# Kernel optimization log

Measured on AMD Instinct MI355X. Metric: run time of the kernel, lower is better.

## Reference

```python
import jax, jax.numpy as jnp
import numpy as np

EPS = 1e-6


def setup_inputs() -> dict:
    key = jax.random.key(0)
    kx, kw = jax.random.split(key)
    B, C, N = 8, 256, 2048
    x = jax.random.normal(kx, (B, C, N), dtype=jnp.float32)
    # nn.Linear(dim*2, 2, bias=False): weight shape [2, 2*C]
    W = jax.random.normal(kw, (2, 2 * C), dtype=jnp.float32) * (1.0 / np.sqrt(2 * C))
    return {"x": x, "W": W}


def reference(x, W):
    B, C, N = x.shape
    # cosine similarity matrix [B, N, N]
    sim = jnp.einsum('bcn,bcm->bnm', x, x)
    # torch: sqrt(sum(x^2 + 1e-6, dim=1)) -> eps added per-channel before sum
    norms = jnp.sqrt(jnp.sum(x * x + EPS, axis=1))            # [B, N]
    io_abs = sim / (norms[:, :, None] * norms[:, None, :])    # [B, N, N]
    # zero the diagonal (fill_diagonal_(0)) before argmax
    io_abs = io_abs * (1.0 - jnp.eye(N, dtype=io_abs.dtype))
    idx = jnp.argmax(io_abs, axis=2)                          # [B, N] nearest-neighbor per token
    # gather retrieved features: f_re[b, :, n] = x[b, :, idx[b, n]]
    f_re = jnp.take_along_axis(x, idx[:, None, :], axis=2)    # [B, C, N]
    # gated fusion
    fus = jnp.concatenate([x, f_re], axis=1).transpose(0, 2, 1)  # [B, N, 2C]
    w = jax.nn.softmax(fus @ W.T, axis=-1)                    # [B, N, 2]
    w = w.transpose(0, 2, 1)                                  # [B, 2, N]
    out = x * w[:, 0:1, :] + f_re * w[:, 1:2, :]
    return (out, f_re)
```

## Files before the change

kernel.cpp:

```cpp
#include <hip/hip_runtime.h>
#include <hip/hip_bf16.h>
#include <math.h>

constexpr int B_ = 8;
constexpr int C_ = 256;
constexpr int N_ = 2048;
constexpr int CN_ = C_ * N_;
constexpr int TOT_ = B_ * C_ * N_;
constexpr int NTILES = 16;
constexpr int NPAIRS = 136;
constexpr float EPSC = 256.0f * 1e-6f;

typedef __attribute__((ext_vector_type(8))) short bf16x8;
typedef __attribute__((ext_vector_type(4))) float f32x4;

__device__ __forceinline__ void g2l16(const void* g, void* l) {
    __builtin_amdgcn_global_load_lds(
        (const __attribute__((address_space(1))) void*)g,
        (__attribute__((address_space(3))) void*)l, 16, 0, 0);
}

__device__ __forceinline__ unsigned short bits(__hip_bfloat16 h) {
    union { __hip_bfloat16 b; unsigned short u; } cv;
    cv.b = h;
    return cv.u;
}

__device__ __forceinline__ float b2f(short s) {
    union { float f; unsigned u; } cv;
    cv.u = ((unsigned)(unsigned short)s) << 16;
    return cv.f;
}

__device__ __forceinline__ unsigned long long packkey(float v, int m) {
    const unsigned b = __float_as_uint(v);
    const unsigned u = (b & 0x80000000u) ? ~b : (b | 0x80000000u);
    return ((unsigned long long)u << 32) | (unsigned)(2047 - m);
}

__global__ __launch_bounds__(256) void convert_kernel(const float* __restrict__ x,
                                                      __hip_bfloat16* __restrict__ hiT,
                                                      __hip_bfloat16* __restrict__ loT,
                                                      float* __restrict__ normacc) {
    const int blk = blockIdx.x;
    const int batch = blk & 7;
    const int nt = (blk >> 3) & 31;
    const int ctile = blk >> 8;
    const int n0 = nt << 6, c0 = ctile << 6;
    const int t = threadIdx.x;
    const int i = t & 63, j = t >> 6;

    __shared__ float tb[64][65];
    __shared__ float red[4][64];

    float s = 0.f;
    const float* xp = x + (size_t)batch * CN_ + (size_t)c0 * N_ + n0 + i;
#pragma unroll 4
    for (int r = 0; r < 16; ++r) {
        const int cl = j + r * 4;
        const float v = xp[(size_t)cl * N_];
        tb[cl][i] = v;
        s += v * v;
    }
    red[j][i] = s;
    __syncthreads();

    const int cp = t & 31;
    const int c2 = cp << 1;
    const int nb = t >> 5;
#pragma unroll 4
    for (int r = 0; r < 8; ++r) {
        const int n = nb + r * 8;
        const float v0 = tb[c2][n], v1 = tb[c2 + 1][n];
        const size_t o = ((size_t)batch * N_ + n0 + n) * C_ + c0 + c2;
        const __hip_bfloat16 h0 = __float2bfloat16(v0);
        const __hip_bfloat16 h1 = __float2bfloat16(v1);
        const __hip_bfloat16 g0 = __float2bfloat16(v0 - __bfloat162float(h0));
        const __hip_bfloat16 g1 = __float2bfloat16(v1 - __bfloat162float(h1));
        ((unsigned*)hiT)[o >> 1] = ((unsigned)bits(h1) << 16) | bits(h0);
        ((unsigned*)loT)[o >> 1] = ((unsigned)bits(g1) << 16) | bits(g0);
    }
    if (j == 0) {
        const float tt = red[0][i] + red[1][i] + red[2][i] + red[3][i];
        atomicAdd(normacc + batch * N_ + n0 + i, tt);
    }
}

__global__ __launch_bounds__(512) void gram_mfma_kernel(
        const __hip_bfloat16* __restrict__ hiT, const __hip_bfloat16* __restrict__ loT,
        const float* __restrict__ normacc,
        float* __restrict__ pval, int* __restrict__ pidx, float* __restrict__ pval2) {
    const int blk = blockIdx.x;
    const int batch = blk & 7;
    int p = blk >> 3;
    int bn = 0;
    while (p >= NTILES - bn) { p -= NTILES - bn; ++bn; }
    const int bm = bn + p;
    const bool diag = (bn == bm);
    const int n0 = bn << 7, m0 = bm << 7;

    __shared__ short As[128 * 64];
    __shared__ short Bs[128 * 64];
    short* ov = &As[0];
    float (*rv1)[4] = (float(*)[4])(ov + 0);
    int (*ri1)[4] = (int(*)[4])(ov + 1024);
    float (*rv2)[4] = (float(*)[4])(ov + 2048);
    float (*cv1)[2] = (float(*)[2])(ov + 3072);
    int (*ci1)[2] = (int(*)[2])(ov + 3584);
    float (*cv2)[2] = (float(*)[2])(ov + 4096);
    float* rnA = (float*)(ov + 4608);

    const int tid = threadIdx.x;
    const int l = tid & 63, w = tid >> 6;
    const int lm = l & 15, q = l >> 4;
    const int x7 = lm & 7;
    const int wn = (w >> 2) << 6;
    const int wm = (w & 3) << 5;

    const size_t bbase = (size_t)batch * CN_;
    const short* gA[2];
    const short* gB[2];
    int ldsoff[2];
#pragma unroll
    for (int pp = 0; pp < 2; ++pp) {
        const int slot = tid + pp * 512;
        const int r = slot >> 3, sidx = slot & 7;
        const int sw = sidx ^ (r & 7);
        const short* base = (const short*)((sw < 4) ? hiT : loT);
        gA[pp] = base + bbase + (size_t)(n0 + r) * C_ + (sw & 3) * 8;
        gB[pp] = base + bbase + (size_t)(m0 + r) * C_ + (sw & 3) * 8;
        ldsoff[pp] = slot * 8;
    }
    int aoff[8], boff[4];
#pragma unroll
    for (int rt = 0; rt < 4; ++rt) {
        const int ra = wn + rt * 16 + lm;
        aoff[rt * 2] = ra * 64 + ((q ^ x7) * 8);
        aoff[rt * 2 + 1] = ra * 64 + (((4 | q) ^ x7) * 8);
    }
#pragma unroll
    for (int ct = 0; ct < 2; ++ct) {
        const int rb = wm + ct * 16 + lm;
        boff[ct * 2] = rb * 64 + ((q ^ x7) * 8);
        boff[ct * 2 + 1] = rb * 64 + (((4 | q) ^ x7) * 8);
    }

    f32x4 acc[4][2];
#pragma unroll
    for (int rt = 0; rt < 4; ++rt)
#pragma unroll
        for (int ct = 0; ct < 2; ++ct) acc[rt][ct] = (f32x4){0.f, 0.f, 0.f, 0.f};

    for (int kt = 0; kt < 8; ++kt) {
        __syncthreads();
#pragma unroll
        for (int pp = 0; pp < 2; ++pp) {
            g2l16(gA[pp] + kt * 32, As + ldsoff[pp]);
            g2l16(gB[pp] + kt * 32, Bs + ldsoff[pp]);
        }
        __syncthreads();
        bf16x8 ah[4], al[4], bh[2], bl[2];
#pragma unroll
        for (int rt = 0; rt < 4; ++rt) {
            ah[rt] = *(const bf16x8*)(As + aoff[rt * 2]);
            al[rt] = *(const bf16x8*)(As + aoff[rt * 2 + 1]);
        }
#pragma unroll
        for (int ct = 0; ct < 2; ++ct) {
            bh[ct] = *(const bf16x8*)(Bs + boff[ct * 2]);
            bl[ct] = *(const bf16x8*)(Bs + boff[ct * 2 + 1]);
        }
#pragma unroll
        for (int rt = 0; rt < 4; ++rt)
#pragma unroll
            for (int ct = 0; ct < 2; ++ct) {
                acc[rt][ct] = __builtin_amdgcn_mfma_f32_16x16x32_bf16(
                    ah[rt], bh[ct], acc[rt][ct], 0, 0, 0);
                acc[rt][ct] = __builtin_amdgcn_mfma_f32_16x16x32_bf16(
                    ah[rt], bl[ct], acc[rt][ct], 0, 0, 0);
                acc[rt][ct] = __builtin_amdgcn_mfma_f32_16x16x32_bf16(
                    al[rt], bh[ct], acc[rt][ct], 0, 0, 0);
            }
    }
    __syncthreads();

    if (tid < 128) rnA[tid] = 1.0f / sqrtf(normacc[batch * N_ + n0 + tid] + EPSC);

    float rnm[2];
#pragma unroll
    for (int ct = 0; ct < 2; ++ct)
        rnm[ct] = 1.0f / sqrtf(normacc[batch * N_ + m0 + wm + ct * 16 + lm] + EPSC);

#pragma unroll
    for (int rt = 0; rt < 4; ++rt) {
#pragma unroll
        for (int r = 0; r < 4; ++r) {
            const int nrow = n0 + wn + rt * 16 + q * 4 + r;
            float v1 = -3.4e38f, v2 = -3.4e38f;
            int i1 = 0x7fffffff;
#pragma unroll
            for (int ct = 0; ct < 2; ++ct) {
                const int m = m0 + wm + ct * 16 + lm;
                const float v = acc[rt][ct][r] * rnm[ct];
                if (m == nrow) continue;
                if (v > v1) { v2 = v1; v1 = v; i1 = m; }
                else if (v > v2) v2 = v;
            }
#pragma unroll
            for (int d = 1; d < 16; d <<= 1) {
                const float ov1 = __shfl_xor(v1, d, 64);
                const int oi1 = __shfl_xor(i1, d, 64);
                const float ov2 = __shfl_xor(v2, d, 64);
                if (ov1 > v1 || (ov1 == v1 && oi1 < i1)) {
                    v2 = fmaxf(v1, ov2); v1 = ov1; i1 = oi1;
                } else {
                    v2 = fmaxf(v2, ov1);
                }
            }
            if (lm == 0) {
                const int rloc = wn + rt * 16 + q * 4 + r;
                rv1[rloc][w & 3] = v1;
                ri1[rloc][w & 3] = i1;
                rv2[rloc][w & 3] = v2;
            }
        }
    }
    __syncthreads();

    if (!diag) {
        float rnn[4][4];
#pragma unroll
        for (int rt = 0; rt < 4; ++rt)
#pragma unroll
            for (int r = 0; r < 4; ++r) rnn[rt][r] = rnA[wn + rt * 16 + q * 4 + r];
#pragma unroll
        for (int ct = 0; ct < 2; ++ct) {
            float v1 = -3.4e38f, v2 = -3.4e38f;
            int i1 = 0x7fffffff;
#pragma unroll
            for (int rt = 0; rt < 4; ++rt) {
#pragma unroll
                for (int r = 0; r < 4; ++r) {
                    const float v = acc[rt][ct][r] * rnn[rt][r];
                    const int nn = n0 + wn + rt * 16 + q * 4 + r;
                    if (v > v1) { v2 = v1; v1 = v; i1 = nn; }
                    else if (v > v2) v2 = v;
                }
            }
#pragma unroll
            for (int d = 16; d < 64; d <<= 1) {
                const float ov1 = __shfl_xor(v1, d, 64);
                const int oi1 = __shfl_xor(i1, d, 64);
                const float ov2 = __shfl_xor(v2, d, 64);
                if (ov1 > v1 || (ov1 == v1 && oi1 < i1)) {
                    v2 = fmaxf(v1, ov2); v1 = ov1; i1 = oi1;
                } else {
                    v2 = fmaxf(v2, ov1);
                }
            }
            if (q == 0) {
                const int mloc = wm + ct * 16 + lm;
                cv1[mloc][w >> 2] = v1;
                ci1[mloc][w >> 2] = i1;
                cv2[mloc][w >> 2] = v2;
            }
        }
    }
    __syncthreads();

    if (tid < 128) {
        {
            float v1 = rv1[tid][0]; int i1 = ri1[tid][0]; float v2 = rv2[tid][0];
#pragma unroll
            for (int s = 1; s < 4; ++s) {
                const float ov1 = rv1[tid][s]; const int oi1 = ri1[tid][s]; const float ov2 = rv2[tid][s];
                if (ov1 > v1 || (ov1 == v1 && oi1 < i1)) { v2 = fmaxf(v1, ov2); v1 = ov1; i1 = oi1; }
                else v2 = fmaxf(v2, ov1);
            }
            const size_t gi = (size_t)(batch * NTILES + bm) * N_ + n0 + tid;
            pval[gi] = v1; pidx[gi] = i1; pval2[gi] = v2;
        }
        if (!diag) {
            float v1 = cv1[tid][0]; int i1 = ci1[tid][0]; float v2 = cv2[tid][0];
            const float ov1 = cv1[tid][1]; const int oi1 = ci1[tid][1]; const float ov2 = cv2[tid][1];
            if (ov1 > v1 || (ov1 == v1 && oi1 < i1)) { v2 = fmaxf(v1, ov2); v1 = ov1; i1 = oi1; }
            else v2 = fmaxf(v2, ov1);
            const size_t gi = (size_t)(batch * NTILES + bn) * N_ + m0 + tid;
            pval[gi] = v1; pidx[gi] = i1; pval2[gi] = v2;
        }
    }
}

__global__ void combine_kernel(const float* __restrict__ pval, const int* __restrict__ pidx,
                               const float* __restrict__ pval2, int* __restrict__ fidx,
                               int* __restrict__ rcnt, int* __restrict__ ridx,
                               unsigned long long* __restrict__ pbest) {
    const int t = blockIdx.x * 256 + threadIdx.x;
    const int batch = t >> 11, n = t & 2047;
    float v1 = -3.4e38f, v2 = -3.4e38f;
    int i1 = 0x7fffffff;
    for (int s = 0; s < NTILES; ++s) {
        const size_t gi = (size_t)(batch * NTILES + s) * N_ + n;
        const float ov1 = pval[gi]; const int oi1 = pidx[gi]; const float ov2 = pval2[gi];
        if (ov1 > v1 || (ov1 == v1 && oi1 < i1)) { v2 = fmaxf(v1, ov2); v1 = ov1; i1 = oi1; }
        else v2 = fmaxf(v2, ov1);
    }
    fidx[t] = i1;
    if (v1 - v2 < 1e-4f) {
        const int slot = atomicAdd(rcnt, 1);
        ridx[slot] = t;
        pbest[slot] = 0ull;
    }
}

__global__ __launch_bounds__(256) void rescue_kernel(const float* __restrict__ x,
                                                     const float* __restrict__ normacc,
                                                     const int* __restrict__ rcnt,
                                                     const int* __restrict__ ridx,
                                                     unsigned long long* __restrict__ pbest) {
    const int cnt = *rcnt;
    const int nwork = cnt << 3;
    const int tid = threadIdx.x;
    __shared__ unsigned long long bk[256];
    for (int wi = blockIdx.x; wi < nwork; wi += gridDim.x) {
        const int rr = wi >> 3, ch = wi & 7;
        const int t = ridx[rr];
        const int batch = t >> 11, n = t & 2047;
        const int m = (ch << 8) + tid;
        const float* xb = x + (size_t)batch * CN_;
        float s0 = 0.f, s1 = 0.f, s2 = 0.f, s3 = 0.f;
        const float* xn = xb + n;
        const float* xm = xb + m;
#pragma unroll 4
        for (int c = 0; c < C_; c += 4) {
            s0 += xn[(size_t)(c + 0) * N_] * xm[(size_t)(c + 0) * N_];
            s1 += xn[(size_t)(c + 1) * N_] * xm[(size_t)(c + 1) * N_];
            s2 += xn[(size_t)(c + 2) * N_] * xm[(size_t)(c + 2) * N_];
            s3 += xn[(size_t)(c + 3) * N_] * xm[(size_t)(c + 3) * N_];
        }
        const float rn = 1.0f / sqrtf(normacc[batch * N_ + m] + EPSC);
        const float v = ((s0 + s1) + (s2 + s3)) * rn;
        bk[tid] = (m == n) ? 0ull : packkey(v, m);
        __syncthreads();
        for (int sft = 128; sft > 0; sft >>= 1) {
            if (tid < sft) {
                const unsigned long long o = bk[tid + sft];
                if (o > bk[tid]) bk[tid] = o;
            }
            __syncthreads();
        }
        if (tid == 0) atomicMax(&pbest[rr], bk[0]);
        __syncthreads();
    }
}

__global__ void rescue_fin_kernel(const unsigned long long* __restrict__ pbest,
                                  const int* __restrict__ rcnt,
                                  const int* __restrict__ ridx,
                                  int* __restrict__ fidx) {
    const int rr = blockIdx.x * 256 + threadIdx.x;
    if (rr < *rcnt) {
        const unsigned long long k = pbest[rr];
        const int m = 2047 - (int)(unsigned)(k & 0xffffffffull);
        fidx[ridx[rr]] = m;
    }
}

__global__ __launch_bounds__(512) void finish_kernel(const float* __restrict__ x,
                                                     const __hip_bfloat16* __restrict__ hiT,
                                                     const __hip_bfloat16* __restrict__ loT,
                                                     const float* __restrict__ W,
                                                     const int* __restrict__ fidx,
                                                     float* __restrict__ out) {
    const int batch = blockIdx.x & 7;
    const int nt = blockIdx.x >> 3;
    const int n0 = nt << 6;
    const int t = threadIdx.x;
    const int lane = t & 63, cw = t >> 6;

    __shared__ float Wl[1024];
    __shared__ int il[64];
    __shared__ float pl0[8][64], pl1[8][64];
    __shared__ float w0s[64], w1s[64];

    for (int u = t; u < 1024; u += 512) Wl[u] = W[u];
    if (t < 64) il[t] = fidx[batch * N_ + n0 + t];
    __syncthreads();

    const int myrow = il[lane];
    const size_t rowb = ((size_t)batch * N_ + myrow) * C_ + cw * 32;

    float fre[32];
    {
        const bf16x8* hp = (const bf16x8*)(hiT + rowb);
        const bf16x8* lp = (const bf16x8*)(loT + rowb);
#pragma unroll
        for (int v8 = 0; v8 < 4; ++v8) {
            const bf16x8 h = hp[v8];
            const bf16x8 g = lp[v8];
#pragma unroll
            for (int e = 0; e < 8; ++e) fre[v8 * 8 + e] = b2f(h[e]) + b2f(g[e]);
        }
    }

    const float* xb = x + (size_t)batch * CN_ + n0 + lane;
    float xr[32];
    float l0 = 0.f, l1 = 0.f;
#pragma unroll
    for (int cc = 0; cc < 32; ++cc) {
        const int c = cw * 32 + cc;
        const float xv = xb[(size_t)c * N_];
        xr[cc] = xv;
        l0 += xv * Wl[c] + fre[cc] * Wl[256 + c];
        l1 += xv * Wl[512 + c] + fre[cc] * Wl[768 + c];
    }
    pl0[cw][lane] = l0;
    pl1[cw][lane] = l1;
    __syncthreads();
    if (t < 64) {
        float L0 = 0.f, L1 = 0.f;
#pragma unroll
        for (int g = 0; g < 8; ++g) { L0 += pl0[g][t]; L1 += pl1[g][t]; }
        const float mx = fmaxf(L0, L1);
        const float e0 = expf(L0 - mx);
        const float e1 = expf(L1 - mx);
        const float inv = 1.0f / (e0 + e1);
        w0s[t] = e0 * inv;
        w1s[t] = e1 * inv;
    }
    __syncthreads();
    const float w0 = w0s[lane], w1 = w1s[lane];

#pragma unroll
    for (int cc = 0; cc < 32; ++cc) {
        const int c = cw * 32 + cc;
        const size_t off = (size_t)batch * CN_ + (size_t)c * N_ + n0 + lane;
        out[off] = xr[cc] * w0 + fre[cc] * w1;
        out[TOT_ + off] = fre[cc];
    }
}

extern "C" void kernel_launch(void* const* d_in, const int* in_sizes, int n_in,
                              void* d_out, int out_size, void* d_ws, size_t ws_size,
                              hipStream_t stream) {
    const float* x = (const float*)d_in[0];
    const float* W = (const float*)d_in[1];
    float* out = (float*)d_out;

    const size_t BF_BYTES = (size_t)TOT_ * 2;
    const size_t NORM_BYTES = (size_t)B_ * N_ * 4;
    const size_t P_BYTES = (size_t)B_ * NTILES * N_ * 4;

    uint8_t* p = (uint8_t*)d_ws;
    __hip_bfloat16* hiT = (__hip_bfloat16*)p; p += BF_BYTES;
    __hip_bfloat16* loT = (__hip_bfloat16*)p; p += BF_BYTES;
    float* normacc = (float*)p; p += NORM_BYTES;
    float* pval = (float*)p; p += P_BYTES;
    int* pidx = (int*)p; p += P_BYTES;
    float* pval2 = (float*)p; p += P_BYTES;
    int* fidx = (int*)p; p += NORM_BYTES;
    int* rcnt = (int*)p; p += 256;
    int* ridx = (int*)p; p += NORM_BYTES;
    unsigned long long* pbest = (unsigned long long*)p; p += (size_t)B_ * N_ * 8;

    hipMemsetAsync(rcnt, 0, 4, stream);
    hipMemsetAsync(normacc, 0, NORM_BYTES, stream);
    convert_kernel<<<1024, 256, 0, stream>>>(x, hiT, loT, normacc);
    gram_mfma_kernel<<<B_ * NPAIRS, 512, 0, stream>>>(hiT, loT, normacc, pval, pidx, pval2);
    combine_kernel<<<64, 256, 0, stream>>>(pval, pidx, pval2, fidx, rcnt, ridx, pbest);
    rescue_kernel<<<256, 256, 0, stream>>>(x, normacc, rcnt, ridx, pbest);
    rescue_fin_kernel<<<64, 256, 0, stream>>>(pbest, rcnt, ridx, fidx);
    finish_kernel<<<256, 512, 0, stream>>>(x, hiT, loT, W, fidx, out);
}
```

Baseline: 184.0 us.

## Double-buffer gram LDS tiles, drop memsets and atomics, fuse rescue finish

The gram kernel now double-buffers its A/B LDS tiles, prefetching the next k-slice while the current one feeds the MFMAs, and needs one barrier per iteration instead of two. Norm partial sums are written per channel tile into four slices and summed by the readers, which removes the atomicAdd and the memset of the accumulator. The rescue counter is zeroed inside convert_kernel instead of by a memset. The rescue_fin kernel is folded into finish_kernel, which scans the rescue list to patch its local indices. Together this cuts two memsets and one launch, at the cost of doubled LDS use (possible occupancy loss) and a per-block scan of the rescue list.

After: 174.2 us. -5.3%, faster.

```diff
diff --git a/kernel.cpp b/kernel.cpp
--- a/kernel.cpp
+++ b/kernel.cpp
@@ -7,6 +7,7 @@
 constexpr int N_ = 2048;
 constexpr int CN_ = C_ * N_;
 constexpr int TOT_ = B_ * C_ * N_;
+constexpr int BN_ = B_ * N_;
 constexpr int NTILES = 16;
 constexpr int NPAIRS = 136;
 constexpr float EPSC = 256.0f * 1e-6f;
@@ -38,10 +39,16 @@
     return ((unsigned long long)u << 32) | (unsigned)(2047 - m);
 }
 
+__device__ __forceinline__ float rnorm4(const float* __restrict__ normp, int idx) {
+    return 1.0f / sqrtf(normp[idx] + normp[BN_ + idx] + normp[2 * BN_ + idx] +
+                        normp[3 * BN_ + idx] + EPSC);
+}
+
 __global__ __launch_bounds__(256) void convert_kernel(const float* __restrict__ x,
                                                       __hip_bfloat16* __restrict__ hiT,
                                                       __hip_bfloat16* __restrict__ loT,
-                                                      float* __restrict__ normacc) {
+                                                      float* __restrict__ normp,
+                                                      int* __restrict__ rcnt) {
     const int blk = blockIdx.x;
     const int batch = blk & 7;
     const int nt = (blk >> 3) & 31;
@@ -49,6 +56,8 @@
     const int n0 = nt << 6, c0 = ctile << 6;
     const int t = threadIdx.x;
     const int i = t & 63, j = t >> 6;
+
+    if (blk == 0 && t == 0) rcnt[0] = 0;
 
     __shared__ float tb[64][65];
     __shared__ float red[4][64];
@@ -82,13 +91,13 @@
     }
     if (j == 0) {
         const float tt = red[0][i] + red[1][i] + red[2][i] + red[3][i];
-        atomicAdd(normacc + batch * N_ + n0 + i, tt);
+        normp[ctile * BN_ + batch * N_ + n0 + i] = tt;
     }
 }
 
 __global__ __launch_bounds__(512) void gram_mfma_kernel(
         const __hip_bfloat16* __restrict__ hiT, const __hip_bfloat16* __restrict__ loT,
-        const float* __restrict__ normacc,
+        const float* __restrict__ normp,
         float* __restrict__ pval, int* __restrict__ pidx, float* __restrict__ pval2) {
     const int blk = blockIdx.x;
     const int batch = blk & 7;
@@ -99,9 +108,11 @@
     const bool diag = (bn == bm);
     const int n0 = bn << 7, m0 = bm << 7;
 
-    __shared__ short As[128 * 64];
-    __shared__ short Bs[128 * 64];
-    short* ov = &As[0];
+    __shared__ short As0[128 * 64];
+    __shared__ short As1[128 * 64];
+    __shared__ short Bs0[128 * 64];
+    __shared__ short Bs1[128 * 64];
+    short* ov = &As0[0];
     float (*rv1)[4] = (float(*)[4])(ov + 0);
     int (*ri1)[4] = (int(*)[4])(ov + 1024);
     float (*rv2)[4] = (float(*)[4])(ov + 2048);
@@ -151,24 +162,36 @@
 #pragma unroll
         for (int ct = 0; ct < 2; ++ct) acc[rt][ct] = (f32x4){0.f, 0.f, 0.f, 0.f};
 
+#pragma unroll
+    for (int pp = 0; pp < 2; ++pp) {
+        g2l16(gA[pp], As0 + ldsoff[pp]);
+        g2l16(gB[pp], Bs0 + ldsoff[pp]);
+    }
+    __syncthreads();
+
+#pragma unroll
     for (int kt = 0; kt < 8; ++kt) {
-        __syncthreads();
-#pragma unroll
-        for (int pp = 0; pp < 2; ++pp) {
-            g2l16(gA[pp] + kt * 32, As + ldsoff[pp]);
-            g2l16(gB[pp] + kt * 32, Bs + ldsoff[pp]);
-        }
-        __syncthreads();
+        short* Ac = (kt & 1) ? As1 : As0;
+        short* Bc = (kt & 1) ? Bs1 : Bs0;
+        if (kt < 7) {
+            short* An = (kt & 1) ? As0 : As1;
+            short* Bn = (kt & 1) ? Bs0 : Bs1;
+#pragma unroll
+            for (int pp = 0; pp < 2; ++pp) {
+                g2l16(gA[pp] + (kt + 1) * 32, An + ldsoff[pp]);
+                g2l16(gB[pp] + (kt + 1) * 32, Bn + ldsoff[pp]);
+            }
+        }
         bf16x8 ah[4], al[4], bh[2], bl[2];
 #pragma unroll
         for (int rt = 0; rt < 4; ++rt) {
-            ah[rt] = *(const bf16x8*)(As + aoff[rt * 2]);
-            al[rt] = *(const bf16x8*)(As + aoff[rt * 2 + 1]);
+            ah[rt] = *(const bf16x8*)(Ac + aoff[rt * 2]);
+            al[rt] = *(const bf16x8*)(Ac + aoff[rt * 2 + 1]);
         }
 #pragma unroll
         for (int ct = 0; ct < 2; ++ct) {
-            bh[ct] = *(const bf16x8*)(Bs + boff[ct * 2]);
-            bl[ct] = *(const bf16x8*)(Bs + boff[ct * 2 + 1]);
+            bh[ct] = *(const bf16x8*)(Bc + boff[ct * 2]);
+            bl[ct] = *(const bf16x8*)(Bc + boff[ct * 2 + 1]);
         }
 #pragma unroll
         for (int rt = 0; rt < 4; ++rt)
@@ -181,15 +204,15 @@
                 acc[rt][ct] = __builtin_amdgcn_mfma_f32_16x16x32_bf16(
                     al[rt], bh[ct], acc[rt][ct], 0, 0, 0);
             }
-    }
-    __syncthreads();
-
-    if (tid < 128) rnA[tid] = 1.0f / sqrtf(normacc[batch * N_ + n0 + tid] + EPSC);
+        __syncthreads();
+    }
+
+    if (tid < 128) rnA[tid] = rnorm4(normp, batch * N_ + n0 + tid);
 
     float rnm[2];
 #pragma unroll
     for (int ct = 0; ct < 2; ++ct)
-        rnm[ct] = 1.0f / sqrtf(normacc[batch * N_ + m0 + wm + ct * 16 + lm] + EPSC);
+        rnm[ct] = rnorm4(normp, batch * N_ + m0 + wm + ct * 16 + lm);
 
 #pragma unroll
     for (int rt = 0; rt < 4; ++rt) {
@@ -314,7 +337,7 @@
 }
 
 __global__ __launch_bounds__(256) void rescue_kernel(const float* __restrict__ x,
-                                                     const float* __restrict__ normacc,
+                                                     const float* __restrict__ normp,
                                                      const int* __restrict__ rcnt,
                                                      const int* __restrict__ ridx,
                                                      unsigned long long* __restrict__ pbest) {
@@ -338,8 +361,7 @@
             s2 += xn[(size_t)(c + 2) * N_] * xm[(size_t)(c + 2) * N_];
             s3 += xn[(size_t)(c + 3) * N_] * xm[(size_t)(c + 3) * N_];
         }
-        const float rn = 1.0f / sqrtf(normacc[batch * N_ + m] + EPSC);
-        const float v = ((s0 + s1) + (s2 + s3)) * rn;
+        const float v = ((s0 + s1) + (s2 + s3)) * rnorm4(normp, batch * N_ + m);
         bk[tid] = (m == n) ? 0ull : packkey(v, m);
         __syncthreads();
         for (int sft = 128; sft > 0; sft >>= 1) {
@@ -354,23 +376,14 @@
     }
 }
 
-__global__ void rescue_fin_kernel(const unsigned long long* __restrict__ pbest,
-                                  const int* __restrict__ rcnt,
-                                  const int* __restrict__ ridx,
-                                  int* __restrict__ fidx) {
-    const int rr = blockIdx.x * 256 + threadIdx.x;
-    if (rr < *rcnt) {
-        const unsigned long long k = pbest[rr];
-        const int m = 2047 - (int)(unsigned)(k & 0xffffffffull);
-        fidx[ridx[rr]] = m;
-    }
-}
-
 __global__ __launch_bounds__(512) void finish_kernel(const float* __restrict__ x,
                                                      const __hip_bfloat16* __restrict__ hiT,
                                                      const __hip_bfloat16* __restrict__ loT,
                                                      const float* __restrict__ W,
                                                      const int* __restrict__ fidx,
+                                                     const int* __restrict__ rcnt,
+                                                     const int* __restrict__ ridx,
+                                                     const unsigned long long* __restrict__ pbest,
                                                      float* __restrict__ out) {
     const int batch = blockIdx.x & 7;
     const int nt = blockIdx.x >> 3;
@@ -385,6 +398,20 @@
 
     for (int u = t; u < 1024; u += 512) Wl[u] = W[u];
     if (t < 64) il[t] = fidx[batch * N_ + n0 + t];
+    __syncthreads();
+    {
+        const int cnt = *rcnt;
+        for (int rr = t; rr < cnt; rr += 512) {
+            const int tt = ridx[rr];
+            if ((tt >> 11) == batch) {
+                const int n = tt & 2047;
+                if (n >= n0 && n < n0 + 64) {
+                    const unsigned long long k = pbest[rr];
+                    il[n - n0] = 2047 - (int)(unsigned)(k & 0xffffffffull);
+                }
+            }
+        }
+    }
     __syncthreads();
 
     const int myrow = il[lane];
@@ -448,27 +475,24 @@
     float* out = (float*)d_out;
 
     const size_t BF_BYTES = (size_t)TOT_ * 2;
-    const size_t NORM_BYTES = (size_t)B_ * N_ * 4;
+    const size_t NORM_BYTES = (size_t)BN_ * 4;
     const size_t P_BYTES = (size_t)B_ * NTILES * N_ * 4;
 
     uint8_t* p = (uint8_t*)d_ws;
     __hip_bfloat16* hiT = (__hip_bfloat16*)p; p += BF_BYTES;
     __hip_bfloat16* loT = (__hip_bfloat16*)p; p += BF_BYTES;
-    float* normacc = (float*)p; p += NORM_BYTES;
+    float* normp = (float*)p; p += 4 * NORM_BYTES;
     float* pval = (float*)p; p += P_BYTES;
     int* pidx = (int*)p; p += P_BYTES;
     float* pval2 = (float*)p; p += P_BYTES;
     int* fidx = (int*)p; p += NORM_BYTES;
     int* rcnt = (int*)p; p += 256;
     int* ridx = (int*)p; p += NORM_BYTES;
-    unsigned long long* pbest = (unsigned long long*)p; p += (size_t)B_ * N_ * 8;
-
-    hipMemsetAsync(rcnt, 0, 4, stream);
-    hipMemsetAsync(normacc, 0, NORM_BYTES, stream);
-    convert_kernel<<<1024, 256, 0, stream>>>(x, hiT, loT, normacc);
-    gram_mfma_kernel<<<B_ * NPAIRS, 512, 0, stream>>>(hiT, loT, normacc, pval, pidx, pval2);
+    unsigned long long* pbest = (unsigned long long*)p; p += (size_t)BN_ * 8;
+
+    convert_kernel<<<1024, 256, 0, stream>>>(x, hiT, loT, normp, rcnt);
+    gram_mfma_kernel<<<B_ * NPAIRS, 512, 0, stream>>>(hiT, loT, normp, pval, pidx, pval2);
     combine_kernel<<<64, 256, 0, stream>>>(pval, pidx, pval2, fidx, rcnt, ridx, pbest);
-    rescue_kernel<<<256, 256, 0, stream>>>(x, normacc, rcnt, ridx, pbest);
-    rescue_fin_kernel<<<64, 256, 0, stream>>>(pbest, rcnt, ridx, fidx);
-    finish_kernel<<<256, 512, 0, stream>>>(x, hiT, loT, W, fidx, out);
-}
+    rescue_kernel<<<256, 256, 0, stream>>>(x, normp, rcnt, ridx, pbest);
+    finish_kernel<<<256, 512, 0, stream>>>(x, hiT, loT, W, fidx, rcnt, ridx, pbest, out);
+}
```
